# Performance work log

Hardware: AMD Instinct MI355X
Metric: run time of the kernel (lower is better)

The kernel has to match this reference:

```python
import jax, jax.numpy as jnp
import numpy as np
import math

V, D, L, H, F, MAXLEN = 32000, 1024, 6, 16, 4096, 2048
B, S = 2, 2048
DK = D // H
EPS = 1e-5


def _ln(x, g, b):
    m = jnp.mean(x, axis=-1, keepdims=True)
    v = jnp.mean((x - m) ** 2, axis=-1, keepdims=True)
    return (x - m) / jnp.sqrt(v + EPS) * g + b


def setup_inputs() -> dict:
    key = jax.random.key(0)
    ks = jax.random.split(key, 12)
    std = 0.02
    inp = {
        "tokens": jax.random.randint(ks[0], (B, S), 0, V),
        "tok_emb": jax.random.normal(ks[1], (V, D), jnp.float32) * std,
        "pos_emb": jax.random.normal(ks[2], (MAXLEN, D), jnp.float32) * std,
        "Wq": jax.random.normal(ks[3], (L, D, D), jnp.float32) * std,
        "Wk": jax.random.normal(ks[4], (L, D, D), jnp.float32) * std,
        "Wv": jax.random.normal(ks[5], (L, D, D), jnp.float32) * std,
        "Wo": jax.random.normal(ks[6], (L, D, D), jnp.float32) * std,
        "ln1_g": jnp.ones((L, D), jnp.float32),
        "ln1_b": jnp.zeros((L, D), jnp.float32),
        "ln2_g": jnp.ones((L, D), jnp.float32),
        "ln2_b": jnp.zeros((L, D), jnp.float32),
        "W1": jax.random.normal(ks[7], (L, D, F), jnp.float32) * std,
        "b1": jnp.zeros((L, F), jnp.float32),
        "W2": jax.random.normal(ks[8], (L, F, D), jnp.float32) * std,
        "b2": jnp.zeros((L, D), jnp.float32),
        "lnf_g": jnp.ones((D,), jnp.float32),
        "lnf_b": jnp.zeros((D,), jnp.float32),
        "Wout": jax.random.normal(ks[9], (D, V), jnp.float32) * std,
    }
    return inp


def _block(x, Wq, Wk, Wv, Wo, ln1_g, ln1_b, ln2_g, ln2_b, W1, b1, W2, b2, mask):
    # causal multi-head attention (pre-LN)
    h = _ln(x, ln1_g, ln1_b)
    q = (h @ Wq).reshape(B, S, H, DK)
    k = (h @ Wk).reshape(B, S, H, DK)
    v = (h @ Wv).reshape(B, S, H, DK)
    scores = jnp.einsum("bqhd,bkhd->bhqk", q, k) / math.sqrt(DK)
    scores = jnp.where(mask, scores, -jnp.inf)
    attn = jax.nn.softmax(scores, axis=-1)
    ctx = jnp.einsum("bhqk,bkhd->bqhd", attn, v).reshape(B, S, D)
    x = x + ctx @ Wo
    # feed-forward
    h = _ln(x, ln2_g, ln2_b)
    h = jax.nn.gelu(h @ W1 + b1, approximate=False)
    x = x + h @ W2 + b2
    return x


def reference(tokens, tok_emb, pos_emb, Wq, Wk, Wv, Wo, ln1_g, ln1_b, ln2_g, ln2_b,
              W1, b1, W2, b2, lnf_g, lnf_b, Wout):
    x = tok_emb[tokens] + pos_emb[:S][None, :, :]  # [B,S,D]
    mask = jnp.tril(jnp.ones((S, S), bool))[None, None]  # [1,1,S,S]
    for l in range(L):
        x = _block(x, Wq[l], Wk[l], Wv[l], Wo[l], ln1_g[l], ln1_b[l],
                   ln2_g[l], ln2_b[l], W1[l], b1[l], W2[l], b2[l], mask)
    x = _ln(x, lnf_g, lnf_b)
    return x @ Wout  # [B,S,V] logits
```

## Files before the change

### kernel.cpp

```cpp
#include <hip/hip_runtime.h>
#include <stdint.h>

typedef unsigned short u16;
typedef __bf16 bf16x8 __attribute__((ext_vector_type(8)));
typedef u16   u16x8  __attribute__((ext_vector_type(8)));
typedef float f32x4  __attribute__((ext_vector_type(4)));

#define AS1(p) (const __attribute__((address_space(1))) void*)(p)
#define AS3(p) (__attribute__((address_space(3))) void*)(p)

__device__ __forceinline__ u16 f2b(float f){
  uint32_t u = __builtin_bit_cast(uint32_t, f);
  u = (u + 0x7FFFu + ((u >> 16) & 1u)) >> 16;
  return (u16)u;
}
__device__ __forceinline__ float fexp2(float x){
#if __has_builtin(__builtin_amdgcn_exp2f)
  return __builtin_amdgcn_exp2f(x);
#else
  return exp2f(x);
#endif
}

__global__ __launch_bounds__(256) void embed_k(const int* __restrict__ tokens,
                                               const float* __restrict__ te,
                                               const float* __restrict__ pe,
                                               float* __restrict__ x){
  const int n = blockIdx.x, tid = threadIdx.x;
  const int tok = tokens[n];
  float4 a = *(const float4*)&te[(size_t)tok * 1024 + tid * 4];
  const float4 p = *(const float4*)&pe[(size_t)(n & 2047) * 1024 + tid * 4];
  a.x += p.x; a.y += p.y; a.z += p.z; a.w += p.w;
  *(float4*)&x[(size_t)n * 1024 + tid * 4] = a;
}

__global__ __launch_bounds__(256) void ln_k(const float* __restrict__ x,
                                            const float* __restrict__ g,
                                            const float* __restrict__ b,
                                            u16* __restrict__ h){
  const int row = blockIdx.x, tid = threadIdx.x;
  const float4 v = *(const float4*)&x[(size_t)row * 1024 + tid * 4];
  float s = v.x + v.y + v.z + v.w;
  float q = v.x*v.x + v.y*v.y + v.z*v.z + v.w*v.w;
#pragma unroll
  for (int m = 32; m; m >>= 1){ s += __shfl_xor(s, m); q += __shfl_xor(q, m); }
  __shared__ float ss[4], qq[4];
  if ((tid & 63) == 0){ ss[tid >> 6] = s; qq[tid >> 6] = q; }
  __syncthreads();
  s = ss[0] + ss[1] + ss[2] + ss[3];
  q = qq[0] + qq[1] + qq[2] + qq[3];
  const float mean = s * (1.f/1024.f);
  const float var  = q * (1.f/1024.f) - mean*mean;
  const float rstd = rsqrtf(var + 1e-5f);
  const float4 gv = *(const float4*)&g[tid*4];
  const float4 bv = *(const float4*)&b[tid*4];
  ushort4 o;
  o.x = f2b((v.x-mean)*rstd*gv.x + bv.x);
  o.y = f2b((v.y-mean)*rstd*gv.y + bv.y);
  o.z = f2b((v.z-mean)*rstd*gv.z + bv.z);
  o.w = f2b((v.w-mean)*rstd*gv.w + bv.w);
  *(ushort4*)&h[(size_t)row * 1024 + tid * 4] = o;
}

__device__ __forceinline__ void conv_tile(const float* __restrict__ src,
                                          u16* __restrict__ dst,
                                          int R, int C, int bx, int by,
                                          u16 (*t)[72], int tid){
  const int r0 = by * 64, c0 = bx * 64;
  const int row = tid >> 4, col4 = tid & 15;
#pragma unroll
  for (int p = 0; p < 4; ++p){
    const int r = row + p * 16;
    const float4 v = *(const float4*)&src[(size_t)(r0 + r) * C + c0 + col4 * 4];
    t[r][col4*4+0] = f2b(v.x); t[r][col4*4+1] = f2b(v.y);
    t[r][col4*4+2] = f2b(v.z); t[r][col4*4+3] = f2b(v.w);
  }
  __syncthreads();
#pragma unroll
  for (int p = 0; p < 4; ++p){
    const int rr = row + p * 16;
    ushort4 w;
    w.x = t[col4*4+0][rr]; w.y = t[col4*4+1][rr];
    w.z = t[col4*4+2][rr]; w.w = t[col4*4+3][rr];
    *(ushort4*)&dst[(size_t)(c0 + rr) * R + r0 + col4 * 4] = w;
  }
}

__global__ __launch_bounds__(256) void conv_t(const float* __restrict__ src,
                                              u16* __restrict__ dst,
                                              int R, int C){
  __shared__ u16 t[64][72];
  conv_tile(src, dst, R, C, blockIdx.x, blockIdx.y, t, threadIdx.x);
}

__global__ __launch_bounds__(256) void conv6_k(const float* __restrict__ Wq,
                                               const float* __restrict__ Wk,
                                               const float* __restrict__ Wv,
                                               const float* __restrict__ Wo,
                                               const float* __restrict__ W1,
                                               const float* __restrict__ W2,
                                               u16* __restrict__ qkvT,
                                               u16* __restrict__ woT,
                                               u16* __restrict__ w1T,
                                               u16* __restrict__ w2T){
  __shared__ u16 t[64][72];
  const int id = blockIdx.x;
  const float* src; u16* dst; int R, C, bx, by;
  if (id < 1024){
    R = 1024; C = 1024;
    const int m = id >> 8, tt = id & 255; bx = tt & 15; by = tt >> 4;
    if (m == 0){ src = Wq; dst = qkvT; }
    else if (m == 1){ src = Wk; dst = qkvT + 1048576; }
    else if (m == 2){ src = Wv; dst = qkvT + 2097152; }
    else { src = Wo; dst = woT; }
  } else if (id < 2048){
    const int tt = id - 1024; R = 1024; C = 4096; bx = tt & 63; by = tt >> 6;
    src = W1; dst = w1T;
  } else {
    const int tt = id - 2048; R = 4096; C = 1024; bx = tt & 15; by = tt >> 4;
    src = W2; dst = w2T;
  }
  conv_tile(src, dst, R, C, bx, by, t, threadIdx.x);
}

template<int EPI>
__global__ __launch_bounds__(256) void gemm_bt(const u16* __restrict__ A,
                                               const u16* __restrict__ BT,
                                               void* __restrict__ Cout,
                                               const float* __restrict__ bias,
                                               int M, int N, int K){
  __shared__ __attribute__((aligned(16))) u16 As[128 * 64];
  __shared__ __attribute__((aligned(16))) u16 Bs[128 * 64];
  const int tid = threadIdx.x;
  const int lane = tid & 63, wave = tid >> 6;
  const int m0 = blockIdx.x * 128, n0 = blockIdx.y * 128;
  const int wm = wave >> 1, wn = wave & 1;
  const int l15 = lane & 15, l4 = lane >> 4;

  const int srow = tid >> 3;
  const int skb  = ((tid & 7) ^ (srow & 7)) * 8;
  const u16* Ag = A  + (size_t)(m0 + srow) * K + skb;
  const u16* Bg = BT + (size_t)(n0 + srow) * K + skb;
  char* AsB = (char*)As + wave * 1024;
  char* BsB = (char*)Bs + wave * 1024;

  f32x4 acc[4][4] = {};

  for (int k0 = 0; k0 < K; k0 += 64){
    __syncthreads();
#pragma unroll
    for (int c = 0; c < 4; ++c){
      __builtin_amdgcn_global_load_lds(AS1(Ag + (size_t)(c*32)*K + k0), AS3(AsB + c*4096), 16, 0, 0);
      __builtin_amdgcn_global_load_lds(AS1(Bg + (size_t)(c*32)*K + k0), AS3(BsB + c*4096), 16, 0, 0);
    }
    __syncthreads();
#pragma unroll
    for (int kk = 0; kk < 64; kk += 32){
      const int krd = kk + l4 * 8;
      const int kx  = (lane & 7) * 8;
      bf16x8 af[4], bfv[4];
#pragma unroll
      for (int mi = 0; mi < 4; ++mi){
        const int r = wm*64 + mi*16 + l15;
        af[mi] = *(const bf16x8*)&As[r*64 + (krd ^ kx)];
      }
#pragma unroll
      for (int ni = 0; ni < 4; ++ni){
        const int r = wn*64 + ni*16 + l15;
        bfv[ni] = *(const bf16x8*)&Bs[r*64 + (krd ^ kx)];
      }
#pragma unroll
      for (int mi = 0; mi < 4; ++mi)
#pragma unroll
        for (int ni = 0; ni < 4; ++ni)
          acc[mi][ni] = __builtin_amdgcn_mfma_f32_16x16x32_bf16(af[mi], bfv[ni], acc[mi][ni], 0, 0, 0);
    }
  }

#pragma unroll
  for (int mi = 0; mi < 4; ++mi){
    const int r = m0 + wm*64 + mi*16 + l4*4;
#pragma unroll
    for (int ni = 0; ni < 4; ++ni){
      const int c = n0 + wn*64 + ni*16 + l15;
      const f32x4 a = acc[mi][ni];
      if constexpr (EPI == 0){
        u16* C = (u16*)Cout;
#pragma unroll
        for (int j = 0; j < 4; ++j) C[(size_t)(r+j)*N + c] = f2b(a[j]);
      } else if constexpr (EPI == 1){
        float* C = (float*)Cout;
        const float bb = bias ? bias[c] : 0.f;
#pragma unroll
        for (int j = 0; j < 4; ++j){ const size_t o = (size_t)(r+j)*N + c; C[o] += a[j] + bb; }
      } else if constexpr (EPI == 2){
        u16* C = (u16*)Cout;
        const float bb = bias[c];
#pragma unroll
        for (int j = 0; j < 4; ++j){
          const float xv = a[j] + bb;
          C[(size_t)(r+j)*N + c] = f2b(0.5f * xv * (1.f + erff(xv * 0.70710678118654752f)));
        }
      } else {
        float* C = (float*)Cout;
#pragma unroll
        for (int j = 0; j < 4; ++j) C[(size_t)(r+j)*N + c] = a[j];
      }
    }
  }
}

template<int EPI>
__global__ __launch_bounds__(512) void gemm_bt2(const u16* __restrict__ A,
                                                const u16* __restrict__ BT,
                                                void* __restrict__ Cout,
                                                const float* __restrict__ bias,
                                                int M, int N, int K){
  __shared__ __attribute__((aligned(16))) u16 Ls[3][2][256*32];
  const int tid = threadIdx.x;
  const int lane = tid & 63, wave = tid >> 6;
  const int m0 = blockIdx.x * 256, n0 = blockIdx.y * 256;
  const int wm = wave >> 2, wn = wave & 3;
  const int l15 = lane & 15, l4 = lane >> 4;

  const int su  = (lane >> 3) & 7;
  const int c8  = (lane & 7) ^ su;
  const int rloc= ((lane >> 3) << 1) | (c8 >> 2);
  const int xl  = (c8 & 3) * 8;

  const u16* Asrc = A  + (size_t)(m0 + wave*16 + rloc) * K + xl;
  const u16* Bsrc = BT + (size_t)(n0 + wave*16 + rloc) * K + xl;
  char* lds0 = (char*)&Ls[0][0][0];
  const int wb = wave * 1024;

#define LOFF(r) (((r) >> 1)*64 + (((((((r) & 1) << 2) | l4)) ^ (((r) >> 1) & 7))*8))

#define STG(sb, k0, L) do{ \
    __builtin_amdgcn_global_load_lds(AS1(Asrc + (size_t)((L)*128)*K + (size_t)(k0)), \
        AS3(lds0 + (sb)*32768 +         (L)*8192 + wb), 16, 0, 0); \
    __builtin_amdgcn_global_load_lds(AS1(Bsrc + (size_t)((L)*128)*K + (size_t)(k0)), \
        AS3(lds0 + (sb)*32768 + 16384 + (L)*8192 + wb), 16, 0, 0); \
  }while(0)

  f32x4 acc[8][4] = {};
  const int nt = K >> 5;

  STG(0, 0, 0);  STG(0, 0, 1);
  STG(1, 32, 0); STG(1, 32, 1);
  asm volatile("s_waitcnt vmcnt(4)" ::: "memory");
  __builtin_amdgcn_s_barrier();

  int buf = 0;
  for (int t = 0; t < nt; ++t){
    const u16* LA = &Ls[buf][0][0];
    const u16* LB = &Ls[buf][1][0];
    int sb = buf + 2; if (sb >= 3) sb -= 3;
    const int kn = (t + 2) << 5;
    const bool st = (t + 2) < nt;

    bf16x8 bf[4], af[4];
#pragma unroll
    for (int ni = 0; ni < 4; ++ni)
      bf[ni] = *(const bf16x8*)&LB[LOFF(wn*64 + ni*16 + l15)];
#pragma unroll
    for (int mi = 0; mi < 4; ++mi)
      af[mi] = *(const bf16x8*)&LA[LOFF(wm*128 + mi*16 + l15)];
    if (st) STG(sb, kn, 0);
    __builtin_amdgcn_s_barrier();
    __builtin_amdgcn_s_setprio(1);
#pragma unroll
    for (int mi = 0; mi < 4; ++mi)
#pragma unroll
      for (int ni = 0; ni < 4; ++ni)
        acc[mi][ni] = __builtin_amdgcn_mfma_f32_16x16x32_bf16(af[mi], bf[ni], acc[mi][ni], 0, 0, 0);
    __builtin_amdgcn_s_setprio(0);
    __builtin_amdgcn_s_barrier();

#pragma unroll
    for (int mi = 0; mi < 4; ++mi)
      af[mi] = *(const bf16x8*)&LA[LOFF(wm*128 + (4+mi)*16 + l15)];
    if (st) STG(sb, kn, 1);
    __builtin_amdgcn_s_barrier();
    __builtin_amdgcn_s_setprio(1);
#pragma unroll
    for (int mi = 0; mi < 4; ++mi)
#pragma unroll
      for (int ni = 0; ni < 4; ++ni)
        acc[4+mi][ni] = __builtin_amdgcn_mfma_f32_16x16x32_bf16(af[mi], bf[ni], acc[4+mi][ni], 0, 0, 0);
    __builtin_amdgcn_s_setprio(0);

    if (t < nt - 2){
      asm volatile("s_waitcnt vmcnt(4)" ::: "memory");
      __builtin_amdgcn_s_barrier();
    } else if (t == nt - 2){
      asm volatile("s_waitcnt vmcnt(0)" ::: "memory");
      __builtin_amdgcn_s_barrier();
    }
    buf = buf + 1; if (buf >= 3) buf -= 3;
  }
#undef STG
#undef LOFF

#pragma unroll
  for (int mi = 0; mi < 8; ++mi){
    const int r = m0 + wm*128 + mi*16 + l4*4;
#pragma unroll
    for (int ni = 0; ni < 4; ++ni){
      const int c = n0 + wn*64 + ni*16 + l15;
      const f32x4 a = acc[mi][ni];
      if constexpr (EPI == 0){
        u16* C = (u16*)Cout;
#pragma unroll
        for (int j = 0; j < 4; ++j) C[(size_t)(r+j)*N + c] = f2b(a[j]);
      } else if constexpr (EPI == 2){
        u16* C = (u16*)Cout;
        const float bb = bias[c];
#pragma unroll
        for (int j = 0; j < 4; ++j){
          const float xv = a[j] + bb;
          C[(size_t)(r+j)*N + c] = f2b(0.5f * xv * (1.f + erff(xv * 0.70710678118654752f)));
        }
      } else {
        float* C = (float*)Cout;
#pragma unroll
        for (int j = 0; j < 4; ++j) C[(size_t)(r+j)*N + c] = a[j];
      }
    }
  }
}

__global__ __launch_bounds__(256) void attn_k(const u16* __restrict__ qkv,
                                              u16* __restrict__ ctx){
  __shared__ __attribute__((aligned(16))) u16 Ks[2][64*64];
  __shared__ __attribute__((aligned(16))) u16 Vt[2][64][72];
  __shared__ __attribute__((aligned(16))) u16 Ps[4][16][72];
  const int tid = threadIdx.x, lane = tid & 63, w = tid >> 6;
  const int l15 = lane & 15, l4 = lane >> 4;
  const int b = blockIdx.y >> 4, h = blockIdx.y & 15;
  const int bx = gridDim.x - 1 - blockIdx.x;
  const int q0 = bx * 64;
  const int qw = q0 + w * 16;
  const u16* qb = qkv + (size_t)b * 2048 * 3072 + h * 64;
  const u16* kb = qb + 1024;
  const u16* vb = qb + 2048;

  const bf16x8 qf0 = *(const bf16x8*)&qb[(size_t)(qw + l15) * 3072 + l4 * 8];
  const bf16x8 qf1 = *(const bf16x8*)&qb[(size_t)(qw + l15) * 3072 + 32 + l4 * 8];

  f32x4 o[4] = {};
  float mrun = -__builtin_inff(), lrun = 0.f;
  const float CEXP = 0.18033688f;

  const int T = bx + 1;
  const int vd = tid & 63, vkc = w;

  {
    u16* kd = &Ks[0][0];
#pragma unroll
    for (int s = 0; s < 2; ++s){
      const int r = s*32 + w*8 + (lane >> 3);
      __builtin_amdgcn_global_load_lds(AS1(kb + (size_t)r * 3072 + ((lane & 7) ^ (r & 7)) * 8),
                                       AS3(kd + (s*32 + w*8) * 64), 16, 0, 0);
    }
    u16 vr[16];
#pragma unroll
    for (int i = 0; i < 16; ++i) vr[i] = vb[(size_t)(vkc*16 + i) * 3072 + vd];
    u16x8 va, vb2;
#pragma unroll
    for (int i = 0; i < 8; ++i){ va[i] = vr[i]; vb2[i] = vr[8+i]; }
    *(u16x8*)&Vt[0][vd][vkc*16]     = va;
    *(u16x8*)&Vt[0][vd][vkc*16 + 8] = vb2;
  }
  __syncthreads();

  for (int t = 0; t < T; ++t){
    const int cur = t & 1;
    const int kt = t * 64;

    u16 vr[16];
    if (t + 1 < T){
      const int ktn = kt + 64;
      u16* kd = &Ks[cur ^ 1][0];
#pragma unroll
      for (int s = 0; s < 2; ++s){
        const int r = s*32 + w*8 + (lane >> 3);
        __builtin_amdgcn_global_load_lds(AS1(kb + (size_t)(ktn + r) * 3072 + ((lane & 7) ^ (r & 7)) * 8),
                                         AS3(kd + (s*32 + w*8) * 64), 16, 0, 0);
      }
#pragma unroll
      for (int i = 0; i < 16; ++i) vr[i] = vb[(size_t)(ktn + vkc*16 + i) * 3072 + vd];
    }

    f32x4 st[4] = {};
    __builtin_amdgcn_s_setprio(1);
#pragma unroll
    for (int t4 = 0; t4 < 4; ++t4){
      const int r = t4*16 + l15;
      const int sx = l15 & 7;
      const bf16x8 kf0 = *(const bf16x8*)&Ks[cur][r*64 + ((l4       ^ sx) * 8)];
      const bf16x8 kf1 = *(const bf16x8*)&Ks[cur][r*64 + (((4 + l4) ^ sx) * 8)];
      st[t4] = __builtin_amdgcn_mfma_f32_16x16x32_bf16(kf0, qf0, st[t4], 0, 0, 0);
      st[t4] = __builtin_amdgcn_mfma_f32_16x16x32_bf16(kf1, qf1, st[t4], 0, 0, 0);
    }
    __builtin_amdgcn_s_setprio(0);

    float sv[16];
#pragma unroll
    for (int t4 = 0; t4 < 4; ++t4)
#pragma unroll
      for (int j = 0; j < 4; ++j) sv[t4*4 + j] = st[t4][j];
    if (t == T - 1){
      const int qrow = qw + l15;
#pragma unroll
      for (int t4 = 0; t4 < 4; ++t4)
#pragma unroll
        for (int j = 0; j < 4; ++j){
          const int k = kt + t4*16 + l4*4 + j;
          if (k > qrow) sv[t4*4 + j] = -__builtin_inff();
        }
    }

    float x0 = fmaxf(fmaxf(sv[0],  sv[1]),  sv[2]);
    float x1 = fmaxf(fmaxf(sv[3],  sv[4]),  sv[5]);
    float x2 = fmaxf(fmaxf(sv[6],  sv[7]),  sv[8]);
    float x3 = fmaxf(fmaxf(sv[9],  sv[10]), sv[11]);
    float x4 = fmaxf(fmaxf(sv[12], sv[13]), sv[14]);
    float mt = fmaxf(fmaxf(fmaxf(x0, x1), x2), fmaxf(fmaxf(x3, x4), sv[15]));
    mt = fmaxf(mt, __shfl_xor(mt, 16));
    mt = fmaxf(mt, __shfl_xor(mt, 32));

    if (__any(mt > mrun + 64.f)){
      const float mn = fmaxf(mrun, mt);
      const float sc = fexp2((mrun - mn) * CEXP);
      lrun *= sc;
      mrun = mn;
#pragma unroll
      for (int j = 0; j < 4; ++j){
        const float scj = __shfl(sc, l4*4 + j);
        o[0][j] *= scj; o[1][j] *= scj; o[2][j] *= scj; o[3][j] *= scj;
      }
    }

    const float mb = -mrun * CEXP;
#pragma unroll
    for (int i = 0; i < 16; ++i) sv[i] = fexp2(__builtin_fmaf(sv[i], CEXP, mb));
    {
      float s0 = sv[0]+sv[1], s1 = sv[2]+sv[3], s2 = sv[4]+sv[5], s3 = sv[6]+sv[7];
      float s4 = sv[8]+sv[9], s5 = sv[10]+sv[11], s6 = sv[12]+sv[13], s7 = sv[14]+sv[15];
      float u0 = (s0+s1) + (s2+s3), u1 = (s4+s5) + (s6+s7);
      float rs = u0 + u1;
      rs += __shfl_xor(rs, 16);
      rs += __shfl_xor(rs, 32);
      lrun += rs;
    }

#pragma unroll
    for (int t4 = 0; t4 < 4; ++t4){
      uint32_t pk0, pk1;
      asm("v_cvt_pk_bf16_f32 %0, %1, %2" : "=v"(pk0) : "v"(sv[t4*4+0]), "v"(sv[t4*4+1]));
      asm("v_cvt_pk_bf16_f32 %0, %1, %2" : "=v"(pk1) : "v"(sv[t4*4+2]), "v"(sv[t4*4+3]));
      *(uint32_t*)&Ps[w][l15][t4*16 + l4*4]     = pk0;
      *(uint32_t*)&Ps[w][l15][t4*16 + l4*4 + 2] = pk1;
    }
    const bf16x8 pa0 = *(const bf16x8*)&Ps[w][l15][l4*8];
    const bf16x8 pa1 = *(const bf16x8*)&Ps[w][l15][32 + l4*8];

    __builtin_amdgcn_s_setprio(1);
#pragma unroll
    for (int dt = 0; dt < 4; ++dt){
      const bf16x8 vf0 = *(const bf16x8*)&Vt[cur][dt*16 + l15][l4*8];
      const bf16x8 vf1 = *(const bf16x8*)&Vt[cur][dt*16 + l15][32 + l4*8];
      o[dt] = __builtin_amdgcn_mfma_f32_16x16x32_bf16(pa0, vf0, o[dt], 0, 0, 0);
      o[dt] = __builtin_amdgcn_mfma_f32_16x16x32_bf16(pa1, vf1, o[dt], 0, 0, 0);
    }
    __builtin_amdgcn_s_setprio(0);

    if (t + 1 < T){
      u16x8 va, vb2;
#pragma unroll
      for (int i = 0; i < 8; ++i){ va[i] = vr[i]; vb2[i] = vr[8+i]; }
      *(u16x8*)&Vt[cur ^ 1][vd][vkc*16]     = va;
      *(u16x8*)&Vt[cur ^ 1][vd][vkc*16 + 8] = vb2;
    }
    __syncthreads();
  }

  const float inv = 1.f / lrun;
#pragma unroll
  for (int j = 0; j < 4; ++j){
    const float invj = __shfl(inv, l4*4 + j);
    u16* cb = ctx + (size_t)b * 2048 * 1024 + (size_t)(qw + l4*4 + j) * 1024 + h * 64;
#pragma unroll
    for (int dt = 0; dt < 4; ++dt)
      cb[dt*16 + l15] = f2b(o[dt][j] * invj);
  }
}

extern "C" void kernel_launch(void* const* d_in, const int* in_sizes, int n_in,
                              void* d_out, int out_size, void* d_ws, size_t ws_size,
                              hipStream_t stream){
  const int*   tokens = (const int*)d_in[0];
  const float* tok_emb= (const float*)d_in[1];
  const float* pos_emb= (const float*)d_in[2];
  const float* Wq  = (const float*)d_in[3];
  const float* Wk  = (const float*)d_in[4];
  const float* Wv  = (const float*)d_in[5];
  const float* Wo  = (const float*)d_in[6];
  const float* ln1g= (const float*)d_in[7];
  const float* ln1b= (const float*)d_in[8];
  const float* ln2g= (const float*)d_in[9];
  const float* ln2b= (const float*)d_in[10];
  const float* W1  = (const float*)d_in[11];
  const float* b1  = (const float*)d_in[12];
  const float* W2  = (const float*)d_in[13];
  const float* b2  = (const float*)d_in[14];
  const float* lnfg= (const float*)d_in[15];
  const float* lnfb= (const float*)d_in[16];
  const float* Wout= (const float*)d_in[17];

  char* ws = (char*)d_ws;
  float* x    = (float*)(ws + 0);
  u16*   h    = (u16*)(ws + 16777216);
  u16*   qkv  = (u16*)(ws + 25165824);
  u16*   ctxb = (u16*)(ws + 50331648);
  u16*   h1   = (u16*)(ws + 58720256);
  u16*   wT   = (u16*)(ws + 92274688);
  u16*   wqkvT= wT;
  u16*   woT  = wT + (size_t)3072 * 1024;
  u16*   w1T  = woT + (size_t)1024 * 1024;
  u16*   w2T  = w1T + (size_t)4096 * 1024;
  u16*   woutT= wT;

  embed_k<<<4096, 256, 0, stream>>>(tokens, tok_emb, pos_emb, x);

  for (int l = 0; l < 6; ++l){
    conv6_k<<<3072, 256, 0, stream>>>(Wq + (size_t)l*1048576, Wk + (size_t)l*1048576,
                                      Wv + (size_t)l*1048576, Wo + (size_t)l*1048576,
                                      W1 + (size_t)l*4194304, W2 + (size_t)l*4194304,
                                      wqkvT, woT, w1T, w2T);

    ln_k<<<4096, 256, 0, stream>>>(x, ln1g + l*1024, ln1b + l*1024, h);
    gemm_bt2<0><<<dim3(16,12), 512, 0, stream>>>(h, wqkvT, qkv, nullptr, 4096, 3072, 1024);
    attn_k<<<dim3(32,32), 256, 0, stream>>>(qkv, ctxb);
    gemm_bt<1><<<dim3(32,8), 256, 0, stream>>>(ctxb, woT, x, nullptr, 4096, 1024, 1024);
    ln_k<<<4096, 256, 0, stream>>>(x, ln2g + l*1024, ln2b + l*1024, h);
    gemm_bt2<2><<<dim3(16,16), 512, 0, stream>>>(h, w1T, h1, b1 + l*4096, 4096, 4096, 1024);
    gemm_bt<1><<<dim3(32,8), 256, 0, stream>>>(h1, w2T, x, b2 + l*1024, 4096, 1024, 4096);
  }

  ln_k<<<4096, 256, 0, stream>>>(x, lnfg, lnfb, h);
  conv_t<<<dim3(500,16), 256, 0, stream>>>(Wout, woutT, 1024, 32000);
  gemm_bt2<3><<<dim3(16,125), 512, 0, stream>>>(h, woutT, (float*)d_out, nullptr, 4096, 32000, 1024);
}
```

Measured before the change: 2.374 ms.

## Double attention query tile per block and split GEMM MFMA phases into quarters

The attention kernel now processes 128 query rows per block, 32 per wave as two 16-row sub-tiles. Each K/V tile loaded into LDS is therefore reused by twice as many queries, and the grid is halved. Waves skip fully masked key tiles. Separately, the bt2 GEMM main loop loads A fragments two at a time across four barrier-separated MFMA phases instead of four at a time across two, lowering register pressure at the cost of more barriers. The attention change doubles per-wave registers and leaves fewer blocks to balance the causal workload.

After: 2.248 ms. -5.3%, faster.

```diff
diff --git a/kernel.cpp b/kernel.cpp
--- a/kernel.cpp
+++ b/kernel.cpp
@@ -242,6 +242,13 @@
         AS3(lds0 + (sb)*32768 + 16384 + (L)*8192 + wb), 16, 0, 0); \
   }while(0)
 
+#define MM(mi, a) do{ \
+    acc[mi][0] = __builtin_amdgcn_mfma_f32_16x16x32_bf16((a), bf[0], acc[mi][0], 0, 0, 0); \
+    acc[mi][1] = __builtin_amdgcn_mfma_f32_16x16x32_bf16((a), bf[1], acc[mi][1], 0, 0, 0); \
+    acc[mi][2] = __builtin_amdgcn_mfma_f32_16x16x32_bf16((a), bf[2], acc[mi][2], 0, 0, 0); \
+    acc[mi][3] = __builtin_amdgcn_mfma_f32_16x16x32_bf16((a), bf[3], acc[mi][3], 0, 0, 0); \
+  }while(0)
+
   f32x4 acc[8][4] = {};
   const int nt = K >> 5;
 
@@ -258,35 +265,38 @@
     const int kn = (t + 2) << 5;
     const bool st = (t + 2) < nt;
 
-    bf16x8 bf[4], af[4];
+    bf16x8 bf[4], af0, af1;
 #pragma unroll
     for (int ni = 0; ni < 4; ++ni)
       bf[ni] = *(const bf16x8*)&LB[LOFF(wn*64 + ni*16 + l15)];
-#pragma unroll
-    for (int mi = 0; mi < 4; ++mi)
-      af[mi] = *(const bf16x8*)&LA[LOFF(wm*128 + mi*16 + l15)];
+    af0 = *(const bf16x8*)&LA[LOFF(wm*128 + 0*16 + l15)];
+    af1 = *(const bf16x8*)&LA[LOFF(wm*128 + 1*16 + l15)];
     if (st) STG(sb, kn, 0);
     __builtin_amdgcn_s_barrier();
     __builtin_amdgcn_s_setprio(1);
-#pragma unroll
-    for (int mi = 0; mi < 4; ++mi)
-#pragma unroll
-      for (int ni = 0; ni < 4; ++ni)
-        acc[mi][ni] = __builtin_amdgcn_mfma_f32_16x16x32_bf16(af[mi], bf[ni], acc[mi][ni], 0, 0, 0);
+    MM(0, af0); MM(1, af1);
     __builtin_amdgcn_s_setprio(0);
+
+    af0 = *(const bf16x8*)&LA[LOFF(wm*128 + 2*16 + l15)];
+    af1 = *(const bf16x8*)&LA[LOFF(wm*128 + 3*16 + l15)];
     __builtin_amdgcn_s_barrier();
-
-#pragma unroll
-    for (int mi = 0; mi < 4; ++mi)
-      af[mi] = *(const bf16x8*)&LA[LOFF(wm*128 + (4+mi)*16 + l15)];
+    __builtin_amdgcn_s_setprio(1);
+    MM(2, af0); MM(3, af1);
+    __builtin_amdgcn_s_setprio(0);
+
+    af0 = *(const bf16x8*)&LA[LOFF(wm*128 + 4*16 + l15)];
+    af1 = *(const bf16x8*)&LA[LOFF(wm*128 + 5*16 + l15)];
     if (st) STG(sb, kn, 1);
     __builtin_amdgcn_s_barrier();
     __builtin_amdgcn_s_setprio(1);
-#pragma unroll
-    for (int mi = 0; mi < 4; ++mi)
-#pragma unroll
-      for (int ni = 0; ni < 4; ++ni)
-        acc[4+mi][ni] = __builtin_amdgcn_mfma_f32_16x16x32_bf16(af[mi], bf[ni], acc[4+mi][ni], 0, 0, 0);
+    MM(4, af0); MM(5, af1);
+    __builtin_amdgcn_s_setprio(0);
+
+    af0 = *(const bf16x8*)&LA[LOFF(wm*128 + 6*16 + l15)];
+    af1 = *(const bf16x8*)&LA[LOFF(wm*128 + 7*16 + l15)];
+    __builtin_amdgcn_s_barrier();
+    __builtin_amdgcn_s_setprio(1);
+    MM(6, af0); MM(7, af1);
     __builtin_amdgcn_s_setprio(0);
 
     if (t < nt - 2){
@@ -300,6 +310,7 @@
   }
 #undef STG
 #undef LOFF
+#undef MM
 
 #pragma unroll
   for (int mi = 0; mi < 8; ++mi){
@@ -333,25 +344,28 @@
                                               u16* __restrict__ ctx){
   __shared__ __attribute__((aligned(16))) u16 Ks[2][64*64];
   __shared__ __attribute__((aligned(16))) u16 Vt[2][64][72];
-  __shared__ __attribute__((aligned(16))) u16 Ps[4][16][72];
+  __shared__ __attribute__((aligned(16))) u16 Ps[8][16][72];
   const int tid = threadIdx.x, lane = tid & 63, w = tid >> 6;
   const int l15 = lane & 15, l4 = lane >> 4;
   const int b = blockIdx.y >> 4, h = blockIdx.y & 15;
   const int bx = gridDim.x - 1 - blockIdx.x;
-  const int q0 = bx * 64;
-  const int qw = q0 + w * 16;
+  const int q0 = bx * 128;
+  const int qw = q0 + w * 32;
   const u16* qb = qkv + (size_t)b * 2048 * 3072 + h * 64;
   const u16* kb = qb + 1024;
   const u16* vb = qb + 2048;
 
-  const bf16x8 qf0 = *(const bf16x8*)&qb[(size_t)(qw + l15) * 3072 + l4 * 8];
-  const bf16x8 qf1 = *(const bf16x8*)&qb[(size_t)(qw + l15) * 3072 + 32 + l4 * 8];
-
-  f32x4 o[4] = {};
-  float mrun = -__builtin_inff(), lrun = 0.f;
+  const bf16x8 qa0 = *(const bf16x8*)&qb[(size_t)(qw + l15) * 3072 + l4 * 8];
+  const bf16x8 qa1 = *(const bf16x8*)&qb[(size_t)(qw + l15) * 3072 + 32 + l4 * 8];
+  const bf16x8 qb0 = *(const bf16x8*)&qb[(size_t)(qw + 16 + l15) * 3072 + l4 * 8];
+  const bf16x8 qb1 = *(const bf16x8*)&qb[(size_t)(qw + 16 + l15) * 3072 + 32 + l4 * 8];
+
+  f32x4 oa[4] = {}, ob[4] = {};
+  float mra = -__builtin_inff(), lra = 0.f;
+  float mrb = -__builtin_inff(), lrb = 0.f;
   const float CEXP = 0.18033688f;
 
-  const int T = bx + 1;
+  const int T = 2*bx + 2;
   const int vd = tid & 63, vkc = w;
 
   {
@@ -391,89 +405,150 @@
       for (int i = 0; i < 16; ++i) vr[i] = vb[(size_t)(ktn + vkc*16 + i) * 3072 + vd];
     }
 
-    f32x4 st[4] = {};
-    __builtin_amdgcn_s_setprio(1);
-#pragma unroll
-    for (int t4 = 0; t4 < 4; ++t4){
-      const int r = t4*16 + l15;
-      const int sx = l15 & 7;
-      const bf16x8 kf0 = *(const bf16x8*)&Ks[cur][r*64 + ((l4       ^ sx) * 8)];
-      const bf16x8 kf1 = *(const bf16x8*)&Ks[cur][r*64 + (((4 + l4) ^ sx) * 8)];
-      st[t4] = __builtin_amdgcn_mfma_f32_16x16x32_bf16(kf0, qf0, st[t4], 0, 0, 0);
-      st[t4] = __builtin_amdgcn_mfma_f32_16x16x32_bf16(kf1, qf1, st[t4], 0, 0, 0);
-    }
-    __builtin_amdgcn_s_setprio(0);
-
-    float sv[16];
-#pragma unroll
-    for (int t4 = 0; t4 < 4; ++t4)
-#pragma unroll
-      for (int j = 0; j < 4; ++j) sv[t4*4 + j] = st[t4][j];
-    if (t == T - 1){
-      const int qrow = qw + l15;
-#pragma unroll
-      for (int t4 = 0; t4 < 4; ++t4)
-#pragma unroll
-        for (int j = 0; j < 4; ++j){
-          const int k = kt + t4*16 + l4*4 + j;
-          if (k > qrow) sv[t4*4 + j] = -__builtin_inff();
-        }
-    }
-
-    float x0 = fmaxf(fmaxf(sv[0],  sv[1]),  sv[2]);
-    float x1 = fmaxf(fmaxf(sv[3],  sv[4]),  sv[5]);
-    float x2 = fmaxf(fmaxf(sv[6],  sv[7]),  sv[8]);
-    float x3 = fmaxf(fmaxf(sv[9],  sv[10]), sv[11]);
-    float x4 = fmaxf(fmaxf(sv[12], sv[13]), sv[14]);
-    float mt = fmaxf(fmaxf(fmaxf(x0, x1), x2), fmaxf(fmaxf(x3, x4), sv[15]));
-    mt = fmaxf(mt, __shfl_xor(mt, 16));
-    mt = fmaxf(mt, __shfl_xor(mt, 32));
-
-    if (__any(mt > mrun + 64.f)){
-      const float mn = fmaxf(mrun, mt);
-      const float sc = fexp2((mrun - mn) * CEXP);
-      lrun *= sc;
-      mrun = mn;
-#pragma unroll
-      for (int j = 0; j < 4; ++j){
-        const float scj = __shfl(sc, l4*4 + j);
-        o[0][j] *= scj; o[1][j] *= scj; o[2][j] *= scj; o[3][j] *= scj;
-      }
-    }
-
-    const float mb = -mrun * CEXP;
-#pragma unroll
-    for (int i = 0; i < 16; ++i) sv[i] = fexp2(__builtin_fmaf(sv[i], CEXP, mb));
-    {
-      float s0 = sv[0]+sv[1], s1 = sv[2]+sv[3], s2 = sv[4]+sv[5], s3 = sv[6]+sv[7];
-      float s4 = sv[8]+sv[9], s5 = sv[10]+sv[11], s6 = sv[12]+sv[13], s7 = sv[14]+sv[15];
-      float u0 = (s0+s1) + (s2+s3), u1 = (s4+s5) + (s6+s7);
-      float rs = u0 + u1;
-      rs += __shfl_xor(rs, 16);
-      rs += __shfl_xor(rs, 32);
-      lrun += rs;
-    }
-
-#pragma unroll
-    for (int t4 = 0; t4 < 4; ++t4){
-      uint32_t pk0, pk1;
-      asm("v_cvt_pk_bf16_f32 %0, %1, %2" : "=v"(pk0) : "v"(sv[t4*4+0]), "v"(sv[t4*4+1]));
-      asm("v_cvt_pk_bf16_f32 %0, %1, %2" : "=v"(pk1) : "v"(sv[t4*4+2]), "v"(sv[t4*4+3]));
-      *(uint32_t*)&Ps[w][l15][t4*16 + l4*4]     = pk0;
-      *(uint32_t*)&Ps[w][l15][t4*16 + l4*4 + 2] = pk1;
-    }
-    const bf16x8 pa0 = *(const bf16x8*)&Ps[w][l15][l4*8];
-    const bf16x8 pa1 = *(const bf16x8*)&Ps[w][l15][32 + l4*8];
-
-    __builtin_amdgcn_s_setprio(1);
-#pragma unroll
-    for (int dt = 0; dt < 4; ++dt){
-      const bf16x8 vf0 = *(const bf16x8*)&Vt[cur][dt*16 + l15][l4*8];
-      const bf16x8 vf1 = *(const bf16x8*)&Vt[cur][dt*16 + l15][32 + l4*8];
-      o[dt] = __builtin_amdgcn_mfma_f32_16x16x32_bf16(pa0, vf0, o[dt], 0, 0, 0);
-      o[dt] = __builtin_amdgcn_mfma_f32_16x16x32_bf16(pa1, vf1, o[dt], 0, 0, 0);
-    }
-    __builtin_amdgcn_s_setprio(0);
+    if (kt <= qw + 31){
+      f32x4 sta[4] = {}, stb[4] = {};
+      __builtin_amdgcn_s_setprio(1);
+#pragma unroll
+      for (int t4 = 0; t4 < 4; ++t4){
+        const int r = t4*16 + l15;
+        const int sx = l15 & 7;
+        const bf16x8 kf0 = *(const bf16x8*)&Ks[cur][r*64 + ((l4       ^ sx) * 8)];
+        const bf16x8 kf1 = *(const bf16x8*)&Ks[cur][r*64 + (((4 + l4) ^ sx) * 8)];
+        sta[t4] = __builtin_amdgcn_mfma_f32_16x16x32_bf16(kf0, qa0, sta[t4], 0, 0, 0);
+        sta[t4] = __builtin_amdgcn_mfma_f32_16x16x32_bf16(kf1, qa1, sta[t4], 0, 0, 0);
+        stb[t4] = __builtin_amdgcn_mfma_f32_16x16x32_bf16(kf0, qb0, stb[t4], 0, 0, 0);
+        stb[t4] = __builtin_amdgcn_mfma_f32_16x16x32_bf16(kf1, qb1, stb[t4], 0, 0, 0);
+      }
+      __builtin_amdgcn_s_setprio(0);
+
+      bf16x8 pa0, pa1, pb0, pb1;
+      {
+        float sv[16];
+#pragma unroll
+        for (int t4 = 0; t4 < 4; ++t4)
+#pragma unroll
+          for (int j = 0; j < 4; ++j) sv[t4*4 + j] = sta[t4][j];
+        if (kt + 63 > qw){
+          const int qrow = qw + l15;
+#pragma unroll
+          for (int t4 = 0; t4 < 4; ++t4)
+#pragma unroll
+            for (int j = 0; j < 4; ++j){
+              const int k = kt + t4*16 + l4*4 + j;
+              if (k > qrow) sv[t4*4 + j] = -__builtin_inff();
+            }
+        }
+        float x0 = fmaxf(fmaxf(sv[0],  sv[1]),  sv[2]);
+        float x1 = fmaxf(fmaxf(sv[3],  sv[4]),  sv[5]);
+        float x2 = fmaxf(fmaxf(sv[6],  sv[7]),  sv[8]);
+        float x3 = fmaxf(fmaxf(sv[9],  sv[10]), sv[11]);
+        float x4 = fmaxf(fmaxf(sv[12], sv[13]), sv[14]);
+        float mt = fmaxf(fmaxf(fmaxf(x0, x1), x2), fmaxf(fmaxf(x3, x4), sv[15]));
+        mt = fmaxf(mt, __shfl_xor(mt, 16));
+        mt = fmaxf(mt, __shfl_xor(mt, 32));
+        if (__any(mt > mra + 64.f)){
+          const float mn = fmaxf(mra, mt);
+          const float sc = fexp2((mra - mn) * CEXP);
+          lra *= sc;
+          mra = mn;
+#pragma unroll
+          for (int j = 0; j < 4; ++j){
+            const float scj = __shfl(sc, l4*4 + j);
+            oa[0][j] *= scj; oa[1][j] *= scj; oa[2][j] *= scj; oa[3][j] *= scj;
+          }
+        }
+        const float mb = -mra * CEXP;
+#pragma unroll
+        for (int i = 0; i < 16; ++i) sv[i] = fexp2(__builtin_fmaf(sv[i], CEXP, mb));
+        {
+          float s0 = sv[0]+sv[1], s1 = sv[2]+sv[3], s2 = sv[4]+sv[5], s3 = sv[6]+sv[7];
+          float s4 = sv[8]+sv[9], s5 = sv[10]+sv[11], s6 = sv[12]+sv[13], s7 = sv[14]+sv[15];
+          float rs = (s0+s1) + (s2+s3) + ((s4+s5) + (s6+s7));
+          rs += __shfl_xor(rs, 16);
+          rs += __shfl_xor(rs, 32);
+          lra += rs;
+        }
+#pragma unroll
+        for (int t4 = 0; t4 < 4; ++t4){
+          uint32_t pk0, pk1;
+          asm("v_cvt_pk_bf16_f32 %0, %1, %2" : "=v"(pk0) : "v"(sv[t4*4+0]), "v"(sv[t4*4+1]));
+          asm("v_cvt_pk_bf16_f32 %0, %1, %2" : "=v"(pk1) : "v"(sv[t4*4+2]), "v"(sv[t4*4+3]));
+          *(uint32_t*)&Ps[2*w][l15][t4*16 + l4*4]     = pk0;
+          *(uint32_t*)&Ps[2*w][l15][t4*16 + l4*4 + 2] = pk1;
+        }
+        pa0 = *(const bf16x8*)&Ps[2*w][l15][l4*8];
+        pa1 = *(const bf16x8*)&Ps[2*w][l15][32 + l4*8];
+      }
+      {
+        float sv[16];
+#pragma unroll
+        for (int t4 = 0; t4 < 4; ++t4)
+#pragma unroll
+          for (int j = 0; j < 4; ++j) sv[t4*4 + j] = stb[t4][j];
+        if (kt + 63 > qw + 16){
+          const int qrow = qw + 16 + l15;
+#pragma unroll
+          for (int t4 = 0; t4 < 4; ++t4)
+#pragma unroll
+            for (int j = 0; j < 4; ++j){
+              const int k = kt + t4*16 + l4*4 + j;
+              if (k > qrow) sv[t4*4 + j] = -__builtin_inff();
+            }
+        }
+        float x0 = fmaxf(fmaxf(sv[0],  sv[1]),  sv[2]);
+        float x1 = fmaxf(fmaxf(sv[3],  sv[4]),  sv[5]);
+        float x2 = fmaxf(fmaxf(sv[6],  sv[7]),  sv[8]);
+        float x3 = fmaxf(fmaxf(sv[9],  sv[10]), sv[11]);
+        float x4 = fmaxf(fmaxf(sv[12], sv[13]), sv[14]);
+        float mt = fmaxf(fmaxf(fmaxf(x0, x1), x2), fmaxf(fmaxf(x3, x4), sv[15]));
+        mt = fmaxf(mt, __shfl_xor(mt, 16));
+        mt = fmaxf(mt, __shfl_xor(mt, 32));
+        if (__any(mt > mrb + 64.f)){
+          const float mn = fmaxf(mrb, mt);
+          const float sc = fexp2((mrb - mn) * CEXP);
+          lrb *= sc;
+          mrb = mn;
+#pragma unroll
+          for (int j = 0; j < 4; ++j){
+            const float scj = __shfl(sc, l4*4 + j);
+            ob[0][j] *= scj; ob[1][j] *= scj; ob[2][j] *= scj; ob[3][j] *= scj;
+          }
+        }
+        const float mb = -mrb * CEXP;
+#pragma unroll
+        for (int i = 0; i < 16; ++i) sv[i] = fexp2(__builtin_fmaf(sv[i], CEXP, mb));
+        {
+          float s0 = sv[0]+sv[1], s1 = sv[2]+sv[3], s2 = sv[4]+sv[5], s3 = sv[6]+sv[7];
+          float s4 = sv[8]+sv[9], s5 = sv[10]+sv[11], s6 = sv[12]+sv[13], s7 = sv[14]+sv[15];
+          float rs = (s0+s1) + (s2+s3) + ((s4+s5) + (s6+s7));
+          rs += __shfl_xor(rs, 16);
+          rs += __shfl_xor(rs, 32);
+          lrb += rs;
+        }
+#pragma unroll
+        for (int t4 = 0; t4 < 4; ++t4){
+          uint32_t pk0, pk1;
+          asm("v_cvt_pk_bf16_f32 %0, %1, %2" : "=v"(pk0) : "v"(sv[t4*4+0]), "v"(sv[t4*4+1]));
+          asm("v_cvt_pk_bf16_f32 %0, %1, %2" : "=v"(pk1) : "v"(sv[t4*4+2]), "v"(sv[t4*4+3]));
+          *(uint32_t*)&Ps[2*w+1][l15][t4*16 + l4*4]     = pk0;
+          *(uint32_t*)&Ps[2*w+1][l15][t4*16 + l4*4 + 2] = pk1;
+        }
+        pb0 = *(const bf16x8*)&Ps[2*w+1][l15][l4*8];
+        pb1 = *(const bf16x8*)&Ps[2*w+1][l15][32 + l4*8];
+      }
+
+      __builtin_amdgcn_s_setprio(1);
+#pragma unroll
+      for (int dt = 0; dt < 4; ++dt){
+        const bf16x8 vf0 = *(const bf16x8*)&Vt[cur][dt*16 + l15][l4*8];
+        const bf16x8 vf1 = *(const bf16x8*)&Vt[cur][dt*16 + l15][32 + l4*8];
+        oa[dt] = __builtin_amdgcn_mfma_f32_16x16x32_bf16(pa0, vf0, oa[dt], 0, 0, 0);
+        oa[dt] = __builtin_amdgcn_mfma_f32_16x16x32_bf16(pa1, vf1, oa[dt], 0, 0, 0);
+        ob[dt] = __builtin_amdgcn_mfma_f32_16x16x32_bf16(pb0, vf0, ob[dt], 0, 0, 0);
+        ob[dt] = __builtin_amdgcn_mfma_f32_16x16x32_bf16(pb1, vf1, ob[dt], 0, 0, 0);
+      }
+      __builtin_amdgcn_s_setprio(0);
+    }
 
     if (t + 1 < T){
       u16x8 va, vb2;
@@ -485,14 +560,18 @@
     __syncthreads();
   }
 
-  const float inv = 1.f / lrun;
+  const float inva = 1.f / lra, invb = 1.f / lrb;
 #pragma unroll
   for (int j = 0; j < 4; ++j){
-    const float invj = __shfl(inv, l4*4 + j);
-    u16* cb = ctx + (size_t)b * 2048 * 1024 + (size_t)(qw + l4*4 + j) * 1024 + h * 64;
-#pragma unroll
-    for (int dt = 0; dt < 4; ++dt)
-      cb[dt*16 + l15] = f2b(o[dt][j] * invj);
+    const float ia = __shfl(inva, l4*4 + j);
+    const float ib = __shfl(invb, l4*4 + j);
+    u16* ca = ctx + (size_t)b * 2048 * 1024 + (size_t)(qw + l4*4 + j) * 1024 + h * 64;
+    u16* cb2 = ca + (size_t)16 * 1024;
+#pragma unroll
+    for (int dt = 0; dt < 4; ++dt){
+      ca[dt*16 + l15]  = f2b(oa[dt][j] * ia);
+      cb2[dt*16 + l15] = f2b(ob[dt][j] * ib);
+    }
   }
 }
 
@@ -541,7 +620,7 @@
 
     ln_k<<<4096, 256, 0, stream>>>(x, ln1g + l*1024, ln1b + l*1024, h);
     gemm_bt2<0><<<dim3(16,12), 512, 0, stream>>>(h, wqkvT, qkv, nullptr, 4096, 3072, 1024);
-    attn_k<<<dim3(32,32), 256, 0, stream>>>(qkv, ctxb);
+    attn_k<<<dim3(16,32), 256, 0, stream>>>(qkv, ctxb);
     gemm_bt<1><<<dim3(32,8), 256, 0, stream>>>(ctxb, woT, x, nullptr, 4096, 1024, 1024);
     ln_k<<<4096, 256, 0, stream>>>(x, ln2g + l*1024, ln2b + l*1024, h);
     gemm_bt2<2><<<dim3(16,16), 512, 0, stream>>>(h, w1T, h1, b1 + l*4096, 4096, 4096, 1024);
```
